# Kernel tuning notes

Measured on AMD Instinct MI355X. Metric: run time of the kernel, lower is better.

Reference implementation:

```python
import jax, jax.numpy as jnp
import numpy as np

B, T, C, H = 4, 4096, 1024, 128

def setup_inputs() -> dict:
    key = jax.random.key(0)
    k1, k2, k3, k4 = jax.random.split(key, 4)
    x = jax.random.normal(k1, (B, T, C), dtype=jnp.float32)
    # nn.Linear(embed, head, bias=False): y = x @ W, store W as [C, H]
    s = 1.0 / np.sqrt(C)
    Wk = jax.random.normal(k2, (C, H), dtype=jnp.float32) * s
    Wq = jax.random.normal(k3, (C, H), dtype=jnp.float32) * s
    Wv = jax.random.normal(k4, (C, H), dtype=jnp.float32) * s
    return {"x": x, "Wk": Wk, "Wq": Wq, "Wv": Wv}

def reference(x, Wk, Wq, Wv):
    Bx, Tx, Cx = x.shape
    scale = Wk.shape[1] ** -0.5
    k = x @ Wk  # [B,T,H]
    q = x @ Wq
    v = x @ Wv
    att = jnp.einsum('bth,bsh->bts', q, k) * scale  # [B,T,T]
    causal = jnp.triu(jnp.ones((Tx, Tx), dtype=bool), k=1)
    att = jnp.where(causal, -jnp.inf, att)
    att = jax.nn.softmax(att, axis=-1)
    # dropout is identity in eval mode
    out = jnp.einsum('bts,bsh->bth', att, v)  # [B,T,H]
    return out
```

## Files before the change

### kernel.cpp

```cpp
#include <hip/hip_runtime.h>
#include <stdint.h>
#include <math.h>

#define B_ 4
#define T_ 4096
#define C_ 1024
#define H_ 128

typedef __attribute__((ext_vector_type(8))) short s16x8;
typedef __attribute__((ext_vector_type(4))) float f32x4;

__device__ __forceinline__ unsigned short f2bf(float f) {
    union { float f; unsigned u; } v; v.f = f;
    unsigned r = v.u + 0x7fffu + ((v.u >> 16) & 1u);
    return (unsigned short)(r >> 16);
}

__device__ __forceinline__ s16x8 as_frag(uint4 u) {
    union { uint4 u; s16x8 s; } v; v.u = u; return v.s;
}

#define QSC (0.0883883476f * 1.4426950408f)

__global__ __launch_bounds__(256) void k_wt(const float* __restrict__ Wk,
                                            const float* __restrict__ Wq,
                                            const float* __restrict__ Wv,
                                            unsigned short* __restrict__ Wt) {
    __shared__ float tile[64][65];
    int w = blockIdx.z;
    const float* W = (w == 0) ? Wk : (w == 1) ? Wq : Wv;
    int c0 = blockIdx.x * 64, h0 = blockIdx.y * 64;
    int tid = threadIdx.x;
#pragma unroll
    for (int k = 0; k < 16; k++) {
        int idx = tid + k * 256;
        int r = idx >> 6, c = idx & 63;
        tile[r][c] = W[(size_t)(c0 + r) * H_ + h0 + c];
    }
    __syncthreads();
#pragma unroll
    for (int k = 0; k < 16; k++) {
        int idx = tid + k * 256;
        int hh = idx >> 6, cc = idx & 63;
        Wt[(size_t)(w * H_ + h0 + hh) * C_ + c0 + cc] = f2bf(tile[cc][hh]);
    }
}

__global__ __launch_bounds__(256, 3) void k_qkv(const float* __restrict__ x,
                                                const unsigned short* __restrict__ Wt,
                                                unsigned short* __restrict__ Qb,
                                                unsigned short* __restrict__ Kb,
                                                unsigned short* __restrict__ Vt) {
    __shared__ unsigned short a_lds[2][64 * 72];
    int tid = threadIdx.x;
    int wv = tid >> 6, lane = tid & 63, quad = lane >> 4, lo = lane & 15;
    int r0 = blockIdx.x * 64;
    int cb = blockIdx.y;
    int nt0 = wv * 3;

    f32x4 acc[3][4];
#pragma unroll
    for (int i = 0; i < 3; i++)
#pragma unroll
        for (int j = 0; j < 4; j++) acc[i][j] = (f32x4){0.f, 0.f, 0.f, 0.f};

    const int row_s = tid >> 2;
    const int seg_s = (tid & 3) * 16;
    size_t xbase = (size_t)(r0 + row_s) * C_ + seg_s;

    const unsigned short* wp[3];
#pragma unroll
    for (int nt = 0; nt < 3; nt++)
        wp[nt] = Wt + (size_t)(cb * 192 + (nt0 + nt) * 16 + lo) * C_ + quad * 8;

    auto pack_store = [&](unsigned short* buf, const float4 (&f)[4]) {
        uint4 u0, u1;
        u0.x = (unsigned)f2bf(f[0].x) | ((unsigned)f2bf(f[0].y) << 16);
        u0.y = (unsigned)f2bf(f[0].z) | ((unsigned)f2bf(f[0].w) << 16);
        u0.z = (unsigned)f2bf(f[1].x) | ((unsigned)f2bf(f[1].y) << 16);
        u0.w = (unsigned)f2bf(f[1].z) | ((unsigned)f2bf(f[1].w) << 16);
        u1.x = (unsigned)f2bf(f[2].x) | ((unsigned)f2bf(f[2].y) << 16);
        u1.y = (unsigned)f2bf(f[2].z) | ((unsigned)f2bf(f[2].w) << 16);
        u1.z = (unsigned)f2bf(f[3].x) | ((unsigned)f2bf(f[3].y) << 16);
        u1.w = (unsigned)f2bf(f[3].z) | ((unsigned)f2bf(f[3].w) << 16);
        *(uint4*)&buf[row_s * 72 + seg_s] = u0;
        *(uint4*)&buf[row_s * 72 + seg_s + 8] = u1;
    };
    auto load_x = [&](float4 (&f)[4], int kc) {
        const float* xp = x + xbase + kc * 64;
#pragma unroll
        for (int j = 0; j < 4; j++) f[j] = *(const float4*)(xp + j * 4);
    };

    float4 xr[4];
    load_x(xr, 0);
    pack_store(a_lds[0], xr);
    __syncthreads();

    for (int kc = 0; kc < 16; kc++) {
        const unsigned short* buf = a_lds[kc & 1];
        float4 xn[4];
        if (kc < 15) load_x(xn, kc + 1);
        s16x8 b[3][2];
#pragma unroll
        for (int nt = 0; nt < 3; nt++)
#pragma unroll
            for (int kh = 0; kh < 2; kh++)
                b[nt][kh] = *(const s16x8*)(wp[nt] + kc * 64 + kh * 32);
        s16x8 af[4][2];
#pragma unroll
        for (int mt = 0; mt < 4; mt++)
#pragma unroll
            for (int kh = 0; kh < 2; kh++)
                af[mt][kh] = *(const s16x8*)&buf[(mt * 16 + lo) * 72 + kh * 32 + quad * 8];
#pragma unroll
        for (int nt = 0; nt < 3; nt++)
#pragma unroll
            for (int kh = 0; kh < 2; kh++)
#pragma unroll
                for (int mt = 0; mt < 4; mt++)
                    acc[nt][mt] = __builtin_amdgcn_mfma_f32_16x16x32_bf16(
                        af[mt][kh], b[nt][kh], acc[nt][mt], 0, 0, 0);
        if (kc < 15) pack_store((unsigned short*)a_lds[(kc & 1) ^ 1], xn);
        __syncthreads();
    }

#pragma unroll
    for (int nt = 0; nt < 3; nt++) {
        int col = cb * 192 + (nt0 + nt) * 16 + lo;
        int w = col >> 7, h = col & 127;
#pragma unroll
        for (int mt = 0; mt < 4; mt++) {
            int mrow = r0 + mt * 16 + quad * 4;
            if (w == 2) {
                int b = mrow >> 12, t0 = mrow & 4095;
                int tp = (t0 & ~31) + (((t0 & 15) >> 2) << 3) + (((t0 >> 4) & 1) << 2);
                uint2 pk;
                pk.x = (unsigned)f2bf(acc[nt][mt][0]) | ((unsigned)f2bf(acc[nt][mt][1]) << 16);
                pk.y = (unsigned)f2bf(acc[nt][mt][2]) | ((unsigned)f2bf(acc[nt][mt][3]) << 16);
                *(uint2*)(Vt + (size_t)(b * H_ + h) * T_ + tp) = pk;
            } else if (w == 1) {
                unsigned short* dst = Qb + (size_t)mrow * H_ + h;
#pragma unroll
                for (int r = 0; r < 4; r++)
                    dst[(size_t)r * H_] = f2bf(acc[nt][mt][r] * QSC);
            } else {
                unsigned short* dst = Kb + (size_t)mrow * H_ + h;
#pragma unroll
                for (int r = 0; r < 4; r++)
                    dst[(size_t)r * H_] = f2bf(acc[nt][mt][r]);
            }
        }
    }
}

#define LOAD_KV(kv0)                                                            \
    do {                                                                        \
        const uint4* kg = (const uint4*)(Kb + (size_t)(batch * T_ + (kv0) + srow_k) * H_); \
        pk0 = kg[sseg_k + 0]; pk1 = kg[sseg_k + 1];                             \
        pk2 = kg[sseg_k + 2]; pk3 = kg[sseg_k + 3];                             \
        const uint4* vg = (const uint4*)(Vt + (size_t)(batch * H_ + srow_v) * T_ + (kv0)); \
        pv0 = vg[sseg_v + 0]; pv1 = vg[sseg_v + 1];                             \
        pv2 = vg[sseg_v + 2]; pv3 = vg[sseg_v + 3];                             \
    } while (0)

template <int NSPLIT>
__global__ __launch_bounds__(256, 3) void k_attn(const unsigned short* __restrict__ Qb,
                                                 const unsigned short* __restrict__ Kb,
                                                 const unsigned short* __restrict__ Vt,
                                                 float* __restrict__ Opart,
                                                 float* __restrict__ Mpart,
                                                 float* __restrict__ Lpart,
                                                 float* __restrict__ out) {
    __shared__ uint4 kbuf[64 * 16];
    __shared__ uint4 vbuf[128 * 8];

    int tid = threadIdx.x;
    int wv = tid >> 6, lane = tid & 63, quad = lane >> 4, lo = lane & 15;

    int id = blockIdx.x;
    int qt = 63 - id / (4 * NSPLIT);
    int rem = id % (4 * NSPLIT);
    int batch = rem / NSPLIT;
    int split = rem % NSPLIT;
    int m0 = qt * 64 + wv * 16;
    int query = m0 + lo;

    s16x8 qf[4];
    size_t qrow = (size_t)(batch * T_ + m0 + lo) * H_;
#pragma unroll
    for (int ks = 0; ks < 4; ks++)
        qf[ks] = *(const s16x8*)(Qb + qrow + ks * 32 + quad * 8);

    f32x4 acc_o[8];
#pragma unroll
    for (int o = 0; o < 8; o++) acc_o[o] = (f32x4){0.f, 0.f, 0.f, 0.f};
    float m_i = -INFINITY, l_i = 0.f;

    const int srow_k = tid >> 2, sseg_k = (tid & 3) * 4;
    const int srow_v = tid >> 1, sseg_v = (tid & 1) * 4;

    uint4 pk0, pk1, pk2, pk3, pv0, pv1, pv2, pv3;
    if (split <= qt) LOAD_KV(split * 64);

    for (int t = split; t <= qt; t += NSPLIT) {
        int kv0 = t * 64;
        kbuf[srow_k * 16 + ((sseg_k + 0) ^ (srow_k & 15))] = pk0;
        kbuf[srow_k * 16 + ((sseg_k + 1) ^ (srow_k & 15))] = pk1;
        kbuf[srow_k * 16 + ((sseg_k + 2) ^ (srow_k & 15))] = pk2;
        kbuf[srow_k * 16 + ((sseg_k + 3) ^ (srow_k & 15))] = pk3;
        vbuf[srow_v * 8 + ((sseg_v + 0) ^ (srow_v & 7))] = pv0;
        vbuf[srow_v * 8 + ((sseg_v + 1) ^ (srow_v & 7))] = pv1;
        vbuf[srow_v * 8 + ((sseg_v + 2) ^ (srow_v & 7))] = pv2;
        vbuf[srow_v * 8 + ((sseg_v + 3) ^ (srow_v & 7))] = pv3;
        __syncthreads();
        if (t + NSPLIT <= qt) LOAD_KV((t + NSPLIT) * 64);

        f32x4 s_acc[4];
#pragma unroll
        for (int nt = 0; nt < 4; nt++) s_acc[nt] = (f32x4){0.f, 0.f, 0.f, 0.f};
#pragma unroll
        for (int ks = 0; ks < 4; ks++) {
#pragma unroll
            for (int nt = 0; nt < 4; nt++) {
                s16x8 kf = as_frag(kbuf[(nt * 16 + lo) * 16 + ((ks * 4 + quad) ^ lo)]);
                s_acc[nt] = __builtin_amdgcn_mfma_f32_16x16x32_bf16(kf, qf[ks], s_acc[nt], 0, 0, 0);
            }
        }

        float p[4][4];
        bool diag = (t == qt);
#pragma unroll
        for (int nt = 0; nt < 4; nt++)
#pragma unroll
            for (int r = 0; r < 4; r++) {
                float sv = s_acc[nt][r];
                if (diag && (kv0 + nt * 16 + quad * 4 + r > query)) sv = -INFINITY;
                p[nt][r] = sv;
            }

        float mx = p[0][0];
#pragma unroll
        for (int nt = 0; nt < 4; nt++)
#pragma unroll
            for (int r = 0; r < 4; r++) mx = fmaxf(mx, p[nt][r]);
        mx = fmaxf(mx, __shfl_xor(mx, 16));
        mx = fmaxf(mx, __shfl_xor(mx, 32));
        float mnew = fmaxf(m_i, mx);
        if (__any(mnew > m_i)) {
            float alpha = exp2f(m_i - mnew);
            l_i *= alpha;
            m_i = mnew;
#pragma unroll
            for (int o = 0; o < 8; o++)
#pragma unroll
                for (int r = 0; r < 4; r++) acc_o[o][r] *= alpha;
        }
        float rs = 0.f;
#pragma unroll
        for (int nt = 0; nt < 4; nt++)
#pragma unroll
            for (int r = 0; r < 4; r++) {
                float pv = exp2f(p[nt][r] - mnew);
                p[nt][r] = pv;
                rs += pv;
            }
        rs += __shfl_xor(rs, 16);
        rs += __shfl_xor(rs, 32);
        l_i += rs;

        s16x8 pf[2];
#pragma unroll
        for (int kt = 0; kt < 2; kt++) {
            uint4 u;
            u.x = (__float_as_uint(p[2 * kt][0]) >> 16) | ((__float_as_uint(p[2 * kt][1]) >> 16) << 16);
            u.y = (__float_as_uint(p[2 * kt][2]) >> 16) | ((__float_as_uint(p[2 * kt][3]) >> 16) << 16);
            u.z = (__float_as_uint(p[2 * kt + 1][0]) >> 16) | ((__float_as_uint(p[2 * kt + 1][1]) >> 16) << 16);
            u.w = (__float_as_uint(p[2 * kt + 1][2]) >> 16) | ((__float_as_uint(p[2 * kt + 1][3]) >> 16) << 16);
            pf[kt] = as_frag(u);
        }

#pragma unroll
        for (int kt = 0; kt < 2; kt++)
#pragma unroll
            for (int o = 0; o < 8; o++) {
                int vrow = o * 16 + lo;
                s16x8 vf = as_frag(vbuf[vrow * 8 + ((kt * 4 + quad) ^ (vrow & 7))]);
                acc_o[o] = __builtin_amdgcn_mfma_f32_16x16x32_bf16(vf, pf[kt], acc_o[o], 0, 0, 0);
            }
        __syncthreads();
    }

    int rowg = batch * T_ + m0 + lo;
    if (NSPLIT == 1) {
        float inv = 1.0f / l_i;
#pragma unroll
        for (int o = 0; o < 8; o++) {
            float4 v = {acc_o[o][0] * inv, acc_o[o][1] * inv,
                        acc_o[o][2] * inv, acc_o[o][3] * inv};
            *(float4*)(out + (size_t)rowg * H_ + o * 16 + quad * 4) = v;
        }
    } else {
        float* Op = Opart + (size_t)split * (16384 * 128);
#pragma unroll
        for (int o = 0; o < 8; o++) {
            float4 v = {acc_o[o][0], acc_o[o][1], acc_o[o][2], acc_o[o][3]};
            *(float4*)(Op + (size_t)rowg * H_ + o * 16 + quad * 4) = v;
        }
        if (quad == 0) {
            Mpart[split * 16384 + rowg] = m_i;
            Lpart[split * 16384 + rowg] = l_i;
        }
    }
}

template <int NSPLIT>
__global__ __launch_bounds__(256) void k_comb(const float* __restrict__ Opart,
                                              const float* __restrict__ Mpart,
                                              const float* __restrict__ Lpart,
                                              float* __restrict__ out) {
    int tid = threadIdx.x;
    int row = blockIdx.x * 8 + (tid >> 5);
    int h4 = (tid & 31) * 4;
    float m[NSPLIT], l[NSPLIT];
    float M = -INFINITY;
#pragma unroll
    for (int s = 0; s < NSPLIT; s++) {
        m[s] = Mpart[s * 16384 + row];
        l[s] = Lpart[s * 16384 + row];
        M = fmaxf(M, m[s]);
    }
    float4 o = {0.f, 0.f, 0.f, 0.f};
    float den = 0.f;
#pragma unroll
    for (int s = 0; s < NSPLIT; s++) {
        float w = exp2f(m[s] - M);
        den += w * l[s];
        float4 v = *(const float4*)(Opart + ((size_t)s * 16384 + row) * H_ + h4);
        o.x += w * v.x; o.y += w * v.y; o.z += w * v.z; o.w += w * v.w;
    }
    float inv = 1.0f / den;
    float4 r = {o.x * inv, o.y * inv, o.z * inv, o.w * inv};
    *(float4*)(out + (size_t)row * H_ + h4) = r;
}

extern "C" void kernel_launch(void* const* d_in, const int* in_sizes, int n_in,
                              void* d_out, int out_size, void* d_ws, size_t ws_size,
                              hipStream_t stream) {
    const float* x  = (const float*)d_in[0];
    const float* Wk = (const float*)d_in[1];
    const float* Wq = (const float*)d_in[2];
    const float* Wv = (const float*)d_in[3];
    char* ws = (char*)d_ws;
    unsigned short* Wt = (unsigned short*)ws;
    unsigned short* Qb = (unsigned short*)(ws + (1u << 20));
    unsigned short* Kb = (unsigned short*)(ws + (5u << 20));
    unsigned short* Vt = (unsigned short*)(ws + (9u << 20));
    float* out = (float*)d_out;

    const size_t SPLIT_O = (size_t)16384 * 128 * 4;
    const size_t base = (size_t)13 << 20;
    const size_t need4 = base + 4 * SPLIT_O + 8 * 65536;
    const size_t need2 = base + 2 * SPLIT_O + 4 * 65536;

    k_wt  <<<dim3(16, 2, 3), 256, 0, stream>>>(Wk, Wq, Wv, Wt);
    k_qkv <<<dim3(256, 2), 256, 0, stream>>>(x, Wt, Qb, Kb, Vt);

    if (ws_size >= need4) {
        float* Op = (float*)(ws + base);
        float* Mp = (float*)(ws + base + 4 * SPLIT_O);
        float* Lp = (float*)(ws + base + 4 * SPLIT_O + 4 * 65536);
        k_attn<4><<<1024, 256, 0, stream>>>(Qb, Kb, Vt, Op, Mp, Lp, out);
        k_comb<4><<<2048, 256, 0, stream>>>(Op, Mp, Lp, out);
    } else if (ws_size >= need2) {
        float* Op = (float*)(ws + base);
        float* Mp = (float*)(ws + base + 2 * SPLIT_O);
        float* Lp = (float*)(ws + base + 2 * SPLIT_O + 2 * 65536);
        k_attn<2><<<512, 256, 0, stream>>>(Qb, Kb, Vt, Op, Mp, Lp, out);
        k_comb<2><<<2048, 256, 0, stream>>>(Op, Mp, Lp, out);
    } else {
        k_attn<1><<<256, 256, 0, stream>>>(Qb, Kb, Vt, nullptr, nullptr, nullptr, out);
    }
}
```

Measured before the change: 167.6 us.

## Double query tile per attention block, add 8-way KV split, unroll QKV GEMM

The attention kernel now gives each wave two 16-row query groups (128 queries per block), so every K/V tile staged in LDS feeds twice as many MFMAs. This halves LDS staging and global K/V traffic per query. To keep enough blocks, the split count goes up to 8 when the workspace allows, and launch bounds drop to 2 blocks per CU to make room for the doubled accumulators. Separately, the QKV projection loop is unrolled by two with explicit ping-pong buffers and prefetch of the weight fragments, and -inf initial maxima are replaced by a large negative finite value. The costs are higher register pressure and a larger partial-output buffer for the combine kernel to read.

New measurement: 187.7 us. 1.12x slower.

```diff
diff --git a/kernel.cpp b/kernel.cpp
--- a/kernel.cpp
+++ b/kernel.cpp
@@ -6,6 +6,8 @@
 #define T_ 4096
 #define C_ 1024
 #define H_ 128
+
+#define MNEG (-1e30f)
 
 typedef __attribute__((ext_vector_type(8))) short s16x8;
 typedef __attribute__((ext_vector_type(4))) float f32x4;
@@ -91,22 +93,14 @@
 #pragma unroll
         for (int j = 0; j < 4; j++) f[j] = *(const float4*)(xp + j * 4);
     };
-
-    float4 xr[4];
-    load_x(xr, 0);
-    pack_store(a_lds[0], xr);
-    __syncthreads();
-
-    for (int kc = 0; kc < 16; kc++) {
-        const unsigned short* buf = a_lds[kc & 1];
-        float4 xn[4];
-        if (kc < 15) load_x(xn, kc + 1);
-        s16x8 b[3][2];
+    auto load_b = [&](s16x8 (&b)[3][2], int kc) {
 #pragma unroll
         for (int nt = 0; nt < 3; nt++)
 #pragma unroll
             for (int kh = 0; kh < 2; kh++)
                 b[nt][kh] = *(const s16x8*)(wp[nt] + kc * 64 + kh * 32);
+    };
+    auto gemm = [&](const unsigned short* buf, const s16x8 (&b)[3][2]) {
         s16x8 af[4][2];
 #pragma unroll
         for (int mt = 0; mt < 4; mt++)
@@ -121,7 +115,26 @@
                 for (int mt = 0; mt < 4; mt++)
                     acc[nt][mt] = __builtin_amdgcn_mfma_f32_16x16x32_bf16(
                         af[mt][kh], b[nt][kh], acc[nt][mt], 0, 0, 0);
-        if (kc < 15) pack_store((unsigned short*)a_lds[(kc & 1) ^ 1], xn);
+    };
+
+    float4 xr[4];
+    s16x8 ba[3][2], bb[3][2];
+    load_x(xr, 0);
+    load_b(ba, 0);
+    pack_store(a_lds[0], xr);
+    __syncthreads();
+
+    for (int kc2 = 0; kc2 < 8; kc2++) {
+        int e = kc2 * 2;
+        float4 xn[4];
+        load_x(xn, e + 1);
+        load_b(bb, e + 1);
+        gemm(a_lds[0], ba);
+        pack_store(a_lds[1], xn);
+        __syncthreads();
+        if (kc2 < 7) { load_x(xn, e + 2); load_b(ba, e + 2); }
+        gemm(a_lds[1], bb);
+        if (kc2 < 7) pack_store(a_lds[0], xn);
         __syncthreads();
     }
 
@@ -165,7 +178,7 @@
     } while (0)
 
 template <int NSPLIT>
-__global__ __launch_bounds__(256, 3) void k_attn(const unsigned short* __restrict__ Qb,
+__global__ __launch_bounds__(256, 2) void k_attn(const unsigned short* __restrict__ Qb,
                                                  const unsigned short* __restrict__ Kb,
                                                  const unsigned short* __restrict__ Vt,
                                                  float* __restrict__ Opart,
@@ -179,31 +192,36 @@
     int wv = tid >> 6, lane = tid & 63, quad = lane >> 4, lo = lane & 15;
 
     int id = blockIdx.x;
-    int qt = 63 - id / (4 * NSPLIT);
+    int qt = 31 - id / (4 * NSPLIT);
     int rem = id % (4 * NSPLIT);
     int batch = rem / NSPLIT;
     int split = rem % NSPLIT;
-    int m0 = qt * 64 + wv * 16;
-    int query = m0 + lo;
-
-    s16x8 qf[4];
-    size_t qrow = (size_t)(batch * T_ + m0 + lo) * H_;
-#pragma unroll
-    for (int ks = 0; ks < 4; ks++)
-        qf[ks] = *(const s16x8*)(Qb + qrow + ks * 32 + quad * 8);
-
-    f32x4 acc_o[8];
-#pragma unroll
-    for (int o = 0; o < 8; o++) acc_o[o] = (f32x4){0.f, 0.f, 0.f, 0.f};
-    float m_i = -INFINITY, l_i = 0.f;
+    int m0 = qt * 128 + wv * 32;
+    int tmax = 2 * qt + 1;
+
+    s16x8 qf[2][4];
+#pragma unroll
+    for (int g = 0; g < 2; g++) {
+        size_t qrow = (size_t)(batch * T_ + m0 + 16 * g + lo) * H_;
+#pragma unroll
+        for (int ks = 0; ks < 4; ks++)
+            qf[g][ks] = *(const s16x8*)(Qb + qrow + ks * 32 + quad * 8);
+    }
+
+    f32x4 acc_o[2][8];
+#pragma unroll
+    for (int g = 0; g < 2; g++)
+#pragma unroll
+        for (int o = 0; o < 8; o++) acc_o[g][o] = (f32x4){0.f, 0.f, 0.f, 0.f};
+    float m_i[2] = {MNEG, MNEG}, l_i[2] = {0.f, 0.f};
 
     const int srow_k = tid >> 2, sseg_k = (tid & 3) * 4;
     const int srow_v = tid >> 1, sseg_v = (tid & 1) * 4;
 
     uint4 pk0, pk1, pk2, pk3, pv0, pv1, pv2, pv3;
-    if (split <= qt) LOAD_KV(split * 64);
-
-    for (int t = split; t <= qt; t += NSPLIT) {
+    if (split <= tmax) LOAD_KV(split * 64);
+
+    for (int t = split; t <= tmax; t += NSPLIT) {
         int kv0 = t * 64;
         kbuf[srow_k * 16 + ((sseg_k + 0) ^ (srow_k & 15))] = pk0;
         kbuf[srow_k * 16 + ((sseg_k + 1) ^ (srow_k & 15))] = pk1;
@@ -214,70 +232,88 @@
         vbuf[srow_v * 8 + ((sseg_v + 2) ^ (srow_v & 7))] = pv2;
         vbuf[srow_v * 8 + ((sseg_v + 3) ^ (srow_v & 7))] = pv3;
         __syncthreads();
-        if (t + NSPLIT <= qt) LOAD_KV((t + NSPLIT) * 64);
-
-        f32x4 s_acc[4];
-#pragma unroll
-        for (int nt = 0; nt < 4; nt++) s_acc[nt] = (f32x4){0.f, 0.f, 0.f, 0.f};
+        if (t + NSPLIT <= tmax) LOAD_KV((t + NSPLIT) * 64);
+
+        f32x4 s_acc[2][4];
+#pragma unroll
+        for (int g = 0; g < 2; g++)
+#pragma unroll
+            for (int nt = 0; nt < 4; nt++) s_acc[g][nt] = (f32x4){0.f, 0.f, 0.f, 0.f};
 #pragma unroll
         for (int ks = 0; ks < 4; ks++) {
 #pragma unroll
             for (int nt = 0; nt < 4; nt++) {
                 s16x8 kf = as_frag(kbuf[(nt * 16 + lo) * 16 + ((ks * 4 + quad) ^ lo)]);
-                s_acc[nt] = __builtin_amdgcn_mfma_f32_16x16x32_bf16(kf, qf[ks], s_acc[nt], 0, 0, 0);
-            }
-        }
-
-        float p[4][4];
-        bool diag = (t == qt);
-#pragma unroll
-        for (int nt = 0; nt < 4; nt++)
-#pragma unroll
-            for (int r = 0; r < 4; r++) {
-                float sv = s_acc[nt][r];
-                if (diag && (kv0 + nt * 16 + quad * 4 + r > query)) sv = -INFINITY;
-                p[nt][r] = sv;
-            }
-
-        float mx = p[0][0];
-#pragma unroll
-        for (int nt = 0; nt < 4; nt++)
-#pragma unroll
-            for (int r = 0; r < 4; r++) mx = fmaxf(mx, p[nt][r]);
-        mx = fmaxf(mx, __shfl_xor(mx, 16));
-        mx = fmaxf(mx, __shfl_xor(mx, 32));
-        float mnew = fmaxf(m_i, mx);
-        if (__any(mnew > m_i)) {
-            float alpha = exp2f(m_i - mnew);
-            l_i *= alpha;
-            m_i = mnew;
-#pragma unroll
-            for (int o = 0; o < 8; o++)
-#pragma unroll
-                for (int r = 0; r < 4; r++) acc_o[o][r] *= alpha;
-        }
-        float rs = 0.f;
-#pragma unroll
-        for (int nt = 0; nt < 4; nt++)
-#pragma unroll
-            for (int r = 0; r < 4; r++) {
-                float pv = exp2f(p[nt][r] - mnew);
-                p[nt][r] = pv;
-                rs += pv;
-            }
-        rs += __shfl_xor(rs, 16);
-        rs += __shfl_xor(rs, 32);
-        l_i += rs;
-
-        s16x8 pf[2];
-#pragma unroll
-        for (int kt = 0; kt < 2; kt++) {
-            uint4 u;
-            u.x = (__float_as_uint(p[2 * kt][0]) >> 16) | ((__float_as_uint(p[2 * kt][1]) >> 16) << 16);
-            u.y = (__float_as_uint(p[2 * kt][2]) >> 16) | ((__float_as_uint(p[2 * kt][3]) >> 16) << 16);
-            u.z = (__float_as_uint(p[2 * kt + 1][0]) >> 16) | ((__float_as_uint(p[2 * kt + 1][1]) >> 16) << 16);
-            u.w = (__float_as_uint(p[2 * kt + 1][2]) >> 16) | ((__float_as_uint(p[2 * kt + 1][3]) >> 16) << 16);
-            pf[kt] = as_frag(u);
+                s_acc[0][nt] = __builtin_amdgcn_mfma_f32_16x16x32_bf16(kf, qf[0][ks], s_acc[0][nt], 0, 0, 0);
+                s_acc[1][nt] = __builtin_amdgcn_mfma_f32_16x16x32_bf16(kf, qf[1][ks], s_acc[1][nt], 0, 0, 0);
+            }
+        }
+
+        float p[2][4][4];
+        bool diag = (t >= 2 * qt);
+#pragma unroll
+        for (int g = 0; g < 2; g++) {
+            int query = m0 + 16 * g + lo;
+#pragma unroll
+            for (int nt = 0; nt < 4; nt++)
+#pragma unroll
+                for (int r = 0; r < 4; r++) {
+                    float sv = s_acc[g][nt][r];
+                    if (diag && (kv0 + nt * 16 + quad * 4 + r > query)) sv = -INFINITY;
+                    p[g][nt][r] = sv;
+                }
+        }
+
+        float mnew[2];
+        bool upd = false;
+#pragma unroll
+        for (int g = 0; g < 2; g++) {
+            float mx = p[g][0][0];
+#pragma unroll
+            for (int nt = 0; nt < 4; nt++)
+#pragma unroll
+                for (int r = 0; r < 4; r++) mx = fmaxf(mx, p[g][nt][r]);
+            mx = fmaxf(mx, __shfl_xor(mx, 16));
+            mx = fmaxf(mx, __shfl_xor(mx, 32));
+            mnew[g] = fmaxf(m_i[g], mx);
+            upd |= (mnew[g] > m_i[g]);
+        }
+        if (__any(upd)) {
+#pragma unroll
+            for (int g = 0; g < 2; g++) {
+                float alpha = exp2f(m_i[g] - mnew[g]);
+                l_i[g] *= alpha;
+                m_i[g] = mnew[g];
+#pragma unroll
+                for (int o = 0; o < 8; o++)
+#pragma unroll
+                    for (int r = 0; r < 4; r++) acc_o[g][o][r] *= alpha;
+            }
+        }
+        s16x8 pf[2][2];
+#pragma unroll
+        for (int g = 0; g < 2; g++) {
+            float rs = 0.f;
+#pragma unroll
+            for (int nt = 0; nt < 4; nt++)
+#pragma unroll
+                for (int r = 0; r < 4; r++) {
+                    float pv = exp2f(p[g][nt][r] - mnew[g]);
+                    p[g][nt][r] = pv;
+                    rs += pv;
+                }
+            rs += __shfl_xor(rs, 16);
+            rs += __shfl_xor(rs, 32);
+            l_i[g] += rs;
+#pragma unroll
+            for (int kt = 0; kt < 2; kt++) {
+                uint4 u;
+                u.x = (__float_as_uint(p[g][2 * kt][0]) >> 16) | ((__float_as_uint(p[g][2 * kt][1]) >> 16) << 16);
+                u.y = (__float_as_uint(p[g][2 * kt][2]) >> 16) | ((__float_as_uint(p[g][2 * kt][3]) >> 16) << 16);
+                u.z = (__float_as_uint(p[g][2 * kt + 1][0]) >> 16) | ((__float_as_uint(p[g][2 * kt + 1][1]) >> 16) << 16);
+                u.w = (__float_as_uint(p[g][2 * kt + 1][2]) >> 16) | ((__float_as_uint(p[g][2 * kt + 1][3]) >> 16) << 16);
+                pf[g][kt] = as_frag(u);
+            }
         }
 
 #pragma unroll
@@ -286,30 +322,34 @@
             for (int o = 0; o < 8; o++) {
                 int vrow = o * 16 + lo;
                 s16x8 vf = as_frag(vbuf[vrow * 8 + ((kt * 4 + quad) ^ (vrow & 7))]);
-                acc_o[o] = __builtin_amdgcn_mfma_f32_16x16x32_bf16(vf, pf[kt], acc_o[o], 0, 0, 0);
+                acc_o[0][o] = __builtin_amdgcn_mfma_f32_16x16x32_bf16(vf, pf[0][kt], acc_o[0][o], 0, 0, 0);
+                acc_o[1][o] = __builtin_amdgcn_mfma_f32_16x16x32_bf16(vf, pf[1][kt], acc_o[1][o], 0, 0, 0);
             }
         __syncthreads();
     }
 
-    int rowg = batch * T_ + m0 + lo;
-    if (NSPLIT == 1) {
-        float inv = 1.0f / l_i;
-#pragma unroll
-        for (int o = 0; o < 8; o++) {
-            float4 v = {acc_o[o][0] * inv, acc_o[o][1] * inv,
-                        acc_o[o][2] * inv, acc_o[o][3] * inv};
-            *(float4*)(out + (size_t)rowg * H_ + o * 16 + quad * 4) = v;
-        }
-    } else {
-        float* Op = Opart + (size_t)split * (16384 * 128);
-#pragma unroll
-        for (int o = 0; o < 8; o++) {
-            float4 v = {acc_o[o][0], acc_o[o][1], acc_o[o][2], acc_o[o][3]};
-            *(float4*)(Op + (size_t)rowg * H_ + o * 16 + quad * 4) = v;
-        }
-        if (quad == 0) {
-            Mpart[split * 16384 + rowg] = m_i;
-            Lpart[split * 16384 + rowg] = l_i;
+#pragma unroll
+    for (int g = 0; g < 2; g++) {
+        int rowg = batch * T_ + m0 + 16 * g + lo;
+        if (NSPLIT == 1) {
+            float inv = 1.0f / l_i[g];
+#pragma unroll
+            for (int o = 0; o < 8; o++) {
+                float4 v = {acc_o[g][o][0] * inv, acc_o[g][o][1] * inv,
+                            acc_o[g][o][2] * inv, acc_o[g][o][3] * inv};
+                *(float4*)(out + (size_t)rowg * H_ + o * 16 + quad * 4) = v;
+            }
+        } else {
+            float* Op = Opart + (size_t)split * (16384 * 128);
+#pragma unroll
+            for (int o = 0; o < 8; o++) {
+                float4 v = {acc_o[g][o][0], acc_o[g][o][1], acc_o[g][o][2], acc_o[g][o][3]};
+                *(float4*)(Op + (size_t)rowg * H_ + o * 16 + quad * 4) = v;
+            }
+            if (quad == 0) {
+                Mpart[split * 16384 + rowg] = m_i[g];
+                Lpart[split * 16384 + rowg] = l_i[g];
+            }
         }
     }
 }
@@ -323,7 +363,7 @@
     int row = blockIdx.x * 8 + (tid >> 5);
     int h4 = (tid & 31) * 4;
     float m[NSPLIT], l[NSPLIT];
-    float M = -INFINITY;
+    float M = MNEG;
 #pragma unroll
     for (int s = 0; s < NSPLIT; s++) {
         m[s] = Mpart[s * 16384 + row];
@@ -360,25 +400,32 @@
 
     const size_t SPLIT_O = (size_t)16384 * 128 * 4;
     const size_t base = (size_t)13 << 20;
+    const size_t need8 = base + 8 * SPLIT_O + 16 * 65536;
     const size_t need4 = base + 4 * SPLIT_O + 8 * 65536;
     const size_t need2 = base + 2 * SPLIT_O + 4 * 65536;
 
     k_wt  <<<dim3(16, 2, 3), 256, 0, stream>>>(Wk, Wq, Wv, Wt);
     k_qkv <<<dim3(256, 2), 256, 0, stream>>>(x, Wt, Qb, Kb, Vt);
 
-    if (ws_size >= need4) {
+    if (ws_size >= need8) {
+        float* Op = (float*)(ws + base);
+        float* Mp = (float*)(ws + base + 8 * SPLIT_O);
+        float* Lp = (float*)(ws + base + 8 * SPLIT_O + 8 * 65536);
+        k_attn<8><<<1024, 256, 0, stream>>>(Qb, Kb, Vt, Op, Mp, Lp, out);
+        k_comb<8><<<2048, 256, 0, stream>>>(Op, Mp, Lp, out);
+    } else if (ws_size >= need4) {
         float* Op = (float*)(ws + base);
         float* Mp = (float*)(ws + base + 4 * SPLIT_O);
         float* Lp = (float*)(ws + base + 4 * SPLIT_O + 4 * 65536);
-        k_attn<4><<<1024, 256, 0, stream>>>(Qb, Kb, Vt, Op, Mp, Lp, out);
+        k_attn<4><<<512, 256, 0, stream>>>(Qb, Kb, Vt, Op, Mp, Lp, out);
         k_comb<4><<<2048, 256, 0, stream>>>(Op, Mp, Lp, out);
     } else if (ws_size >= need2) {
         float* Op = (float*)(ws + base);
         float* Mp = (float*)(ws + base + 2 * SPLIT_O);
         float* Lp = (float*)(ws + base + 2 * SPLIT_O + 2 * 65536);
-        k_attn<2><<<512, 256, 0, stream>>>(Qb, Kb, Vt, Op, Mp, Lp, out);
+        k_attn<2><<<256, 256, 0, stream>>>(Qb, Kb, Vt, Op, Mp, Lp, out);
         k_comb<2><<<2048, 256, 0, stream>>>(Op, Mp, Lp, out);
     } else {
-        k_attn<1><<<256, 256, 0, stream>>>(Qb, Kb, Vt, nullptr, nullptr, nullptr, out);
-    }
-}
+        k_attn<1><<<128, 256, 0, stream>>>(Qb, Kb, Vt, nullptr, nullptr, nullptr, out);
+    }
+}
```

## Deepen QKV projection pipeline with two-stage register prefetch and relax occupancy

Applied to the files above, without the earlier changes.

Restructures the QKV projection main loop into a two-step unrolled pipeline. Each step prefetches x two chunks ahead and the weight fragments one chunk ahead into registers, and packs the next LDS buffer before running the MFMAs on the current one. This should hide more global-load latency. It lowers the launch_bounds occupancy hint from 3 to 2 so the extra live registers fit. It also swaps -INFINITY for a large negative finite constant as the initial running max in the attention and combine kernels, which avoids inf arithmetic in exp2.

After: 173.3 us. 1.03x slower.

```diff
diff --git a/kernel.cpp b/kernel.cpp
--- a/kernel.cpp
+++ b/kernel.cpp
@@ -6,6 +6,8 @@
 #define T_ 4096
 #define C_ 1024
 #define H_ 128
+
+#define MNEG (-1e30f)
 
 typedef __attribute__((ext_vector_type(8))) short s16x8;
 typedef __attribute__((ext_vector_type(4))) float f32x4;
@@ -46,7 +48,7 @@
     }
 }
 
-__global__ __launch_bounds__(256, 3) void k_qkv(const float* __restrict__ x,
+__global__ __launch_bounds__(256, 2) void k_qkv(const float* __restrict__ x,
                                                 const unsigned short* __restrict__ Wt,
                                                 unsigned short* __restrict__ Qb,
                                                 unsigned short* __restrict__ Kb,
@@ -91,22 +93,14 @@
 #pragma unroll
         for (int j = 0; j < 4; j++) f[j] = *(const float4*)(xp + j * 4);
     };
-
-    float4 xr[4];
-    load_x(xr, 0);
-    pack_store(a_lds[0], xr);
-    __syncthreads();
-
-    for (int kc = 0; kc < 16; kc++) {
-        const unsigned short* buf = a_lds[kc & 1];
-        float4 xn[4];
-        if (kc < 15) load_x(xn, kc + 1);
-        s16x8 b[3][2];
+    auto load_b = [&](s16x8 (&b)[3][2], int kc) {
 #pragma unroll
         for (int nt = 0; nt < 3; nt++)
 #pragma unroll
             for (int kh = 0; kh < 2; kh++)
                 b[nt][kh] = *(const s16x8*)(wp[nt] + kc * 64 + kh * 32);
+    };
+    auto gemm = [&](const unsigned short* buf, const s16x8 (&b)[3][2]) {
         s16x8 af[4][2];
 #pragma unroll
         for (int mt = 0; mt < 4; mt++)
@@ -121,7 +115,29 @@
                 for (int mt = 0; mt < 4; mt++)
                     acc[nt][mt] = __builtin_amdgcn_mfma_f32_16x16x32_bf16(
                         af[mt][kh], b[nt][kh], acc[nt][mt], 0, 0, 0);
-        if (kc < 15) pack_store((unsigned short*)a_lds[(kc & 1) ^ 1], xn);
+    };
+
+    float4 xa[4], xb[4];
+    s16x8 ba[3][2], bb[3][2];
+    load_x(xa, 0);
+    load_x(xb, 1);
+    load_b(ba, 0);
+    pack_store(a_lds[0], xa);
+    __syncthreads();
+
+    for (int kc2 = 0; kc2 < 8; kc2++) {
+        int e = 2 * kc2;
+        if (e + 2 < 16) load_x(xa, e + 2);
+        load_b(bb, e + 1);
+        pack_store(a_lds[1], xb);
+        gemm(a_lds[0], ba);
+        __syncthreads();
+        if (e + 3 < 16) load_x(xb, e + 3);
+        if (e + 2 < 16) {
+            load_b(ba, e + 2);
+            pack_store(a_lds[0], xa);
+        }
+        gemm(a_lds[1], bb);
         __syncthreads();
     }
 
@@ -195,7 +211,7 @@
     f32x4 acc_o[8];
 #pragma unroll
     for (int o = 0; o < 8; o++) acc_o[o] = (f32x4){0.f, 0.f, 0.f, 0.f};
-    float m_i = -INFINITY, l_i = 0.f;
+    float m_i = MNEG, l_i = 0.f;
 
     const int srow_k = tid >> 2, sseg_k = (tid & 3) * 4;
     const int srow_v = tid >> 1, sseg_v = (tid & 1) * 4;
@@ -323,7 +339,7 @@
     int row = blockIdx.x * 8 + (tid >> 5);
     int h4 = (tid & 31) * 4;
     float m[NSPLIT], l[NSPLIT];
-    float M = -INFINITY;
+    float M = MNEG;
 #pragma unroll
     for (int s = 0; s < NSPLIT; s++) {
         m[s] = Mpart[s * 16384 + row];
```
